# Kernel tuning notes

Hardware: AMD Instinct MI355X
Metric: run time of the kernel (lower is better)

Reference implementation:

```python
import jax, jax.numpy as jnp
import numpy as np

# ---- model / data constants ----
B, N, D, L = 32, 96, 64, 5          # graphs, nodes per graph, hidden, layers
EP = 768                             # directed edges per graph (symmetrized in to_dense)
NODE_VOCAB = 11                      # matches LocalFWL2(..., 11, 5, 'instance')
EDGE_VOCAB = 5                       # edge labels 0..4; index 5 = 'no edge' embedding row
EPS = 1e-5


def setup_inputs() -> dict:
    key = jax.random.key(0)
    ks = jax.random.split(key, 12)
    # block-contiguous batch: graph b owns nodes [b*N, (b+1)*N)
    x = jax.random.randint(ks[0], (B * N,), 0, NODE_VOCAB)
    u = jax.random.randint(ks[1], (B, EP), 0, N)
    v = jax.random.randint(ks[2], (B, EP), 0, N)
    off = (jnp.arange(B) * N)[:, None]
    edge_index = jnp.stack([(u + off).reshape(-1), (v + off).reshape(-1)], axis=0)
    edge_attr = jax.random.randint(ks[3], (B * EP,), 0, EDGE_VOCAB)
    s = 0.1
    inv = 1.0 / np.sqrt(D)
    return {
        "x": x,
        "edge_index": edge_index,
        "edge_attr": edge_attr,
        "node_emb": jax.random.normal(ks[4], (NODE_VOCAB, D), jnp.float32) * s,
        "edge_emb": jax.random.normal(ks[5], (EDGE_VOCAB + 1, D), jnp.float32) * s,
        "W1": jax.random.normal(ks[6], (L, D, D), jnp.float32) * inv,
        "b1": jnp.zeros((L, D), jnp.float32),
        "W2": jax.random.normal(ks[7], (L, D, D), jnp.float32) * inv,
        "b2": jnp.zeros((L, D), jnp.float32),
        "Wm": jax.random.normal(ks[8], (L, D, D), jnp.float32) * inv,
        "bm": jnp.zeros((L, D), jnp.float32),
        "gamma": jnp.ones((L, D), jnp.float32),
        "beta": jnp.zeros((L, D), jnp.float32),
        "pool_w": jax.random.normal(ks[9], (D, 1), jnp.float32) * inv,
        "pool_b": jnp.zeros((1,), jnp.float32),
    }


def reference(x, edge_index, edge_attr, node_emb, edge_emb,
              W1, b1, W2, b2, Wm, bm, gamma, beta, pool_w, pool_b):
    # ---- to_dense: sparse edge list -> dense per-graph edge-label matrix ----
    g = edge_index[0] // N
    u = edge_index[0] % N
    v = edge_index[1] % N
    A = jnp.full((B, N, N), EDGE_VOCAB, dtype=jnp.int32)        # EDGE_VOCAB = no-edge
    ea = edge_attr.astype(jnp.int32)
    A = A.at[g, u, v].set(ea)
    A = A.at[g, v, u].set(ea)                                    # undirected
    adj = (A != EDGE_VOCAB).astype(node_emb.dtype)               # [B,N,N]

    # ---- pair-state init: W_uv = h_u + h_v + edge_emb(A_uv) ----
    H = node_emb[x.reshape(B, N)]                                # [B,N,D]
    W = H[:, :, None, :] + H[:, None, :, :] + edge_emb[A]        # [B,N,N,D]

    # ---- local FWL(2) layers ----
    for l in range(L):
        h1 = jax.nn.relu(jnp.einsum('buwd,de->buwe', W, W1[l]) + b1[l])
        h2 = jax.nn.relu(jnp.einsum('bwvd,de->bwve', W, W2[l]) + b2[l])
        # aggregate over w restricted to neighbors of v (local FWL2)
        M = jnp.einsum('buwd,bwv,bwvd->buvd', h1, adj, h2)       # [B,N,N,D]
        W = W + jnp.einsum('buvd,de->buve', M, Wm[l]) + bm[l]
        # instance norm over the pair dims (u,v), per graph, per channel
        mu = W.mean(axis=(1, 2), keepdims=True)
        var = W.var(axis=(1, 2), keepdims=True)
        W = gamma[l] * (W - mu) * jax.lax.rsqrt(var + EPS) + beta[l]
        W = jax.nn.relu(W)

    # ---- pooling: sum over all pairs, then Linear(D, 1), squeeze ----
    pooled = W.sum(axis=(1, 2))                                  # [B,D]
    return (pooled @ pool_w + pool_b).squeeze(-1)                # [B]
```

## Files before the change

### kernel.cpp

```cpp
#include <hip/hip_runtime.h>
#include <hip/hip_bf16.h>

#define B_ 32
#define N_ 96
#define D_ 64
#define L_ 5
#define BE_ 24576
#define NN_ 9216
#define BNN_ 294912
#define EPS_ 1e-5f
#define INV_NN (1.0f/9216.0f)

typedef unsigned short u16;
typedef unsigned int u32;
typedef __attribute__((ext_vector_type(8))) short bf16x8;
typedef __attribute__((ext_vector_type(4))) float f32x4;

__device__ __forceinline__ float bf2f(u16 r){ return __uint_as_float(((u32)r) << 16); }
__device__ __forceinline__ u32 f2bf(float f){
  u32 u = __float_as_uint(f);
  return (u + 0x7fffu + ((u >> 16) & 1u)) >> 16;
}
__device__ __forceinline__ u32 pack2(float lo, float hi){
  return f2bf(lo) | (f2bf(hi) << 16);
}

__global__ void k_scatter(const int* __restrict__ ei, const int* __restrict__ ea,
                          int* __restrict__ A)
{
  int e = blockIdx.x * 256 + threadIdx.x;
  if (e >= BE_) return;
  int a = ei[e], bnode = ei[BE_ + e];
  int g = a / N_;
  int u = a % N_;
  int v = bnode % N_;
  int lab = ea[e] & 7;
  int base = g * NN_;
  atomicMax(&A[base + u * N_ + v], ((e + 1) << 3) | lab);
  atomicMax(&A[base + v * N_ + u], ((BE_ + e + 1) << 3) | lab);
}

__launch_bounds__(256)
__global__ void k_winit(const int* __restrict__ x, const int* __restrict__ A,
                        const float* __restrict__ nemb, const float* __restrict__ eemb,
                        u16* __restrict__ W)
{
  int gid = blockIdx.x * 256 + threadIdx.x;
  int d = (gid & 15) * 4;
  int p = gid >> 4;
  int b = p / NN_;
  int rem = p % NN_;
  int u = rem / N_;
  int v = rem % N_;
  int xu = x[b * N_ + u], xv = x[b * N_ + v];
  int pk = A[p];
  int lab = pk ? (pk & 7) : 5;
  float4 nu = *(const float4*)(nemb + xu * 64 + d);
  float4 nv = *(const float4*)(nemb + xv * 64 + d);
  float4 ee = *(const float4*)(eemb + lab * 64 + d);
  uint2 o;
  o.x = pack2(nu.x + nv.x + ee.x, nu.y + nv.y + ee.y);
  o.y = pack2(nu.z + nv.z + ee.z, nu.w + nv.w + ee.w);
  ((uint2*)W)[gid] = o;
}

__global__ void k_prep(const float* __restrict__ W1, const float* __restrict__ W2,
                       const float* __restrict__ Wm, u16* __restrict__ WT)
{
  int idx = blockIdx.x * 256 + threadIdx.x;
  if (idx >= 15 * 4096) return;
  int l3 = idx >> 12;
  int r  = idx & 4095;
  int e = r >> 6, d = r & 63;
  int l = l3 / 3, which = l3 % 3;
  const float* s = which == 0 ? W1 : which == 1 ? W2 : Wm;
  WT[idx] = (u16)f2bf(s[l * 4096 + d * 64 + e]);
}

__launch_bounds__(256)
__global__ void k_lin2(const u16* __restrict__ W, const u16* __restrict__ WT1,
                       const u16* __restrict__ WT2,
                       const float* __restrict__ b1l, const float* __restrict__ b2l,
                       const int* __restrict__ A,
                       const float* __restrict__ stp, const float* __restrict__ gml,
                       const float* __restrict__ btl,
                       int use_norm, u16* __restrict__ h1, u16* __restrict__ g2)
{
  __shared__ u16 Cs[64 * 136];
  __shared__ float nsS[128];
  const int tid = threadIdx.x;
  const int wave = tid >> 6, lane = tid & 63;
  const int lm = lane & 15, lg = lane >> 4;
  const int b = blockIdx.x / 72;
  const int qbase = (blockIdx.x % 72) * 128;

  if (use_norm) {
    if (tid < 128) nsS[tid] = stp[(size_t)b * 128 + tid];
    __syncthreads();
  }

  float sc[2][8], sh[2][8];
  if (use_norm) {
    #pragma unroll
    for (int s = 0; s < 2; ++s) {
      int d0 = s * 32 + lg * 8;
      #pragma unroll
      for (int j = 0; j < 8; ++j) {
        int d = d0 + j;
        float S1 = nsS[d], S2 = nsS[64 + d];
        float mu = S1 * INV_NN;
        float var = fmaf(S2, INV_NN, -mu * mu);
        float s0 = gml[d] * rsqrtf(var + EPS_);
        sc[s][j] = s0;
        sh[s][j] = fmaf(-mu, s0, btl[d]);
      }
    }
  } else {
    #pragma unroll
    for (int s = 0; s < 2; ++s)
      #pragma unroll
      for (int j = 0; j < 8; ++j) { sc[s][j] = 1.f; sh[s][j] = 0.f; }
  }

  bf16x8 bF[2][2];
  int flags[2];
  #pragma unroll
  for (int qt = 0; qt < 2; ++qt) {
    int q = qbase + wave * 32 + qt * 16 + lm;
    const u16* wrow = W + ((size_t)b * NN_ + q) * 64;
    flags[qt] = A[b * NN_ + q];
    #pragma unroll
    for (int s = 0; s < 2; ++s) {
      bf16x8 raw = *(const bf16x8*)(wrow + s * 32 + lg * 8);
      if (use_norm) {
        bf16x8 bb;
        #pragma unroll
        for (int j = 0; j < 8; ++j) {
          float v = bf2f((u16)raw[j]);
          v = fmaxf(fmaf(v, sc[s][j], sh[s][j]), 0.f);
          bb[j] = (short)f2bf(v);
        }
        bF[qt][s] = bb;
      } else {
        bF[qt][s] = raw;
      }
    }
  }

  const f32x4 zf = {0.f, 0.f, 0.f, 0.f};

  {
    bf16x8 aF[4][2];
    #pragma unroll
    for (int et = 0; et < 4; ++et)
      #pragma unroll
      for (int s = 0; s < 2; ++s)
        aF[et][s] = *(const bf16x8*)(WT1 + (et * 16 + lm) * 64 + s * 32 + lg * 8);
    float4 bsv[4];
    #pragma unroll
    for (int et = 0; et < 4; ++et) bsv[et] = *(const float4*)(b1l + et * 16 + lg * 4);
    #pragma unroll
    for (int qt = 0; qt < 2; ++qt) {
      f32x4 acc[4] = {zf, zf, zf, zf};
      #pragma unroll
      for (int s = 0; s < 2; ++s)
        #pragma unroll
        for (int et = 0; et < 4; ++et)
          acc[et] = __builtin_amdgcn_mfma_f32_16x16x32_bf16(aF[et][s], bF[qt][s], acc[et], 0, 0, 0);
      int col = wave * 32 + qt * 16 + lm;
      #pragma unroll
      for (int et = 0; et < 4; ++et) {
        float bv[4] = {bsv[et].x, bsv[et].y, bsv[et].z, bsv[et].w};
        #pragma unroll
        for (int r = 0; r < 4; ++r)
          Cs[(et * 16 + lg * 4 + r) * 136 + col] = (u16)f2bf(fmaxf(acc[et][r] + bv[r], 0.f));
      }
    }
  }
  __syncthreads();
  {
    u16* ob = h1 + (size_t)b * 64 * NN_ + qbase;
    for (int i = tid; i < 1024; i += 256) {
      int e = i >> 4, qc = (i & 15) * 8;
      uint4 val = *(const uint4*)&Cs[e * 136 + qc];
      *(uint4*)(ob + (size_t)e * NN_ + qc) = val;
    }
  }
  __syncthreads();

  {
    bf16x8 aF[4][2];
    #pragma unroll
    for (int et = 0; et < 4; ++et)
      #pragma unroll
      for (int s = 0; s < 2; ++s)
        aF[et][s] = *(const bf16x8*)(WT2 + (et * 16 + lm) * 64 + s * 32 + lg * 8);
    float4 bsv[4];
    #pragma unroll
    for (int et = 0; et < 4; ++et) bsv[et] = *(const float4*)(b2l + et * 16 + lg * 4);
    #pragma unroll
    for (int qt = 0; qt < 2; ++qt) {
      f32x4 acc[4] = {zf, zf, zf, zf};
      #pragma unroll
      for (int s = 0; s < 2; ++s)
        #pragma unroll
        for (int et = 0; et < 4; ++et)
          acc[et] = __builtin_amdgcn_mfma_f32_16x16x32_bf16(aF[et][s], bF[qt][s], acc[et], 0, 0, 0);
      int col = wave * 32 + qt * 16 + lm;
      #pragma unroll
      for (int et = 0; et < 4; ++et) {
        float bv[4] = {bsv[et].x, bsv[et].y, bsv[et].z, bsv[et].w};
        #pragma unroll
        for (int r = 0; r < 4; ++r) {
          float v = fmaxf(acc[et][r] + bv[r], 0.f);
          if (!flags[qt]) v = 0.f;
          Cs[(et * 16 + lg * 4 + r) * 136 + col] = (u16)f2bf(v);
        }
      }
    }
  }
  __syncthreads();
  {
    u16* ob = g2 + (size_t)b * 64 * NN_ + qbase;
    for (int i = tid; i < 1024; i += 256) {
      int e = i >> 4, qc = (i & 15) * 8;
      uint4 val = *(const uint4*)&Cs[e * 136 + qc];
      *(uint4*)(ob + (size_t)e * NN_ + qc) = val;
    }
  }
}

__launch_bounds__(256, 4)
__global__ void k_einsum(const u16* __restrict__ h1, const u16* __restrict__ g2n,
                         u16* __restrict__ M)
{
  __shared__ u32 Bt[96 * 60];
  u16* Cst = (u16*)Bt;
  const int tid = threadIdx.x;
  const int wave = tid >> 6, lane = tid & 63;
  const int lm = lane & 15, lg = lane >> 4;
  const int bd = blockIdx.x;
  const u16* h1p = h1 + (size_t)bd * NN_;
  const u16* g2p = g2n + (size_t)bd * NN_;
  const int u0 = (wave & 1) * 48, v0 = (wave >> 1) * 48;

  #pragma unroll
  for (int it = 0; it < 9; ++it) {
    int p = it * 256 + tid;
    int wp = p / 48, vh = (p % 48) * 2;
    u32 a = *(const u32*)(g2p + (2 * wp) * 96 + vh);
    u32 c = *(const u32*)(g2p + (2 * wp + 1) * 96 + vh);
    Bt[vh * 60 + wp]       = (a & 0xffffu) | (c << 16);
    Bt[(vh + 1) * 60 + wp] = (a >> 16) | (c & 0xffff0000u);
  }

  bf16x8 aF[3][3];
  #pragma unroll
  for (int t = 0; t < 3; ++t)
    #pragma unroll
    for (int s = 0; s < 3; ++s)
      aF[t][s] = *(const bf16x8*)(h1p + (u0 + t * 16 + lm) * 96 + s * 32 + lg * 8);
  __syncthreads();

  const f32x4 zf = {0.f, 0.f, 0.f, 0.f};
  f32x4 acc[3][3];
  #pragma unroll
  for (int i = 0; i < 3; ++i)
    #pragma unroll
    for (int j = 0; j < 3; ++j) acc[i][j] = zf;

  #pragma unroll
  for (int s = 0; s < 3; ++s) {
    bf16x8 bb[3];
    #pragma unroll
    for (int vt = 0; vt < 3; ++vt)
      bb[vt] = *(const bf16x8*)&Bt[(v0 + vt * 16 + lm) * 60 + s * 16 + lg * 4];
    #pragma unroll
    for (int ut = 0; ut < 3; ++ut)
      #pragma unroll
      for (int vt = 0; vt < 3; ++vt)
        acc[ut][vt] = __builtin_amdgcn_mfma_f32_16x16x32_bf16(aF[ut][s], bb[vt], acc[ut][vt], 0, 0, 0);
  }
  __syncthreads();

  #pragma unroll
  for (int ut = 0; ut < 3; ++ut)
    #pragma unroll
    for (int vt = 0; vt < 3; ++vt)
      #pragma unroll
      for (int r = 0; r < 4; ++r)
        Cst[(u0 + ut * 16 + lg * 4 + r) * 104 + v0 + vt * 16 + lm] = (u16)f2bf(acc[ut][vt][r]);
  __syncthreads();
  u16* Mp = M + (size_t)bd * NN_;
  for (int i = tid; i < 1152; i += 256) {
    int u = i / 12, vc = (i % 12) * 8;
    uint4 val = *(const uint4*)&Cst[u * 104 + vc];
    *(uint4*)(Mp + u * 96 + vc) = val;
  }
}

__launch_bounds__(128)
__global__ void k_update(const u16* __restrict__ M, const u16* __restrict__ WmT,
                         const float* __restrict__ bml, u16* __restrict__ W,
                         const float* __restrict__ stp, const float* __restrict__ gml,
                         const float* __restrict__ btl, int use_norm,
                         float* __restrict__ sto)
{
  __shared__ u16 Mt[64 * 64];
  __shared__ float red[2][128];
  __shared__ float nsS[128];
  const int tid = threadIdx.x;
  const int wave = tid >> 6, lane = tid & 63;
  const int lm = lane & 15, lg = lane >> 4;
  const int b = blockIdx.x / 144;
  const int qi = blockIdx.x % 144;
  const int qblk = qi * 64;

  if (use_norm) {
    if (tid < 128) nsS[tid] = stp[(size_t)b * 128 + tid];
  }

  bf16x8 aF[4][2];
  #pragma unroll
  for (int et = 0; et < 4; ++et)
    #pragma unroll
    for (int s = 0; s < 2; ++s)
      aF[et][s] = *(const bf16x8*)(WmT + (et * 16 + lm) * 64 + s * 32 + lg * 8);

  uint2 wres[2][4];
  #pragma unroll
  for (int qtL = 0; qtL < 2; ++qtL) {
    int qg = qblk + (wave * 2 + qtL) * 16 + lm;
    const u16* Wp = W + ((size_t)b * NN_ + qg) * 64;
    #pragma unroll
    for (int et = 0; et < 4; ++et)
      wres[qtL][et] = *(const uint2*)(Wp + et * 16 + lg * 4);
  }

  {
    const int dpl = tid >> 1;
    const int qob = tid & 1;
    const u16* Mb = M + (size_t)(b * 64 + dpl) * NN_ + qblk;
    #pragma unroll
    for (int t = 0; t < 4; ++t) {
      int qo = qob + t * 2;
      uint4 v = *(const uint4*)(Mb + qo * 8);
      u32 ws[4] = {v.x, v.y, v.z, v.w};
      #pragma unroll
      for (int h = 0; h < 4; ++h) {
        int j0 = h * 2;
        int q0 = qo * 8 + j0;
        int slot0 = (dpl >> 3) ^ j0 ^ (qo & 7);
        int slot1 = (dpl >> 3) ^ (j0 + 1) ^ (qo & 7);
        Mt[q0 * 64 + slot0 * 8 + (dpl & 7)]       = (u16)(ws[h] & 0xffffu);
        Mt[(q0 + 1) * 64 + slot1 * 8 + (dpl & 7)] = (u16)(ws[h] >> 16);
      }
    }
  }
  __syncthreads();

  float scn[4][4], shn[4][4];
  if (use_norm) {
    #pragma unroll
    for (int et = 0; et < 4; ++et) {
      int e0 = et * 16 + lg * 4;
      #pragma unroll
      for (int r = 0; r < 4; ++r) {
        int e = e0 + r;
        float S1 = nsS[e], S2 = nsS[64 + e];
        float mu = S1 * INV_NN;
        float var = fmaf(S2, INV_NN, -mu * mu);
        float s0 = gml[e] * rsqrtf(var + EPS_);
        scn[et][r] = s0;
        shn[et][r] = fmaf(-mu, s0, btl[e]);
      }
    }
  } else {
    #pragma unroll
    for (int et = 0; et < 4; ++et)
      #pragma unroll
      for (int r = 0; r < 4; ++r) { scn[et][r] = 1.f; shn[et][r] = 0.f; }
  }

  const f32x4 zf = {0.f, 0.f, 0.f, 0.f};
  f32x4 acc[2][4];
  #pragma unroll
  for (int i = 0; i < 2; ++i)
    #pragma unroll
    for (int j = 0; j < 4; ++j) acc[i][j] = zf;

  #pragma unroll
  for (int qtL = 0; qtL < 2; ++qtL) {
    int ql = (wave * 2 + qtL) * 16 + lm;
    bf16x8 bF[2];
    #pragma unroll
    for (int s = 0; s < 2; ++s) {
      int slot = (s * 4 + lg) ^ (ql & 7) ^ ((ql >> 3) & 7);
      bF[s] = *(const bf16x8*)&Mt[ql * 64 + slot * 8];
    }
    #pragma unroll
    for (int s = 0; s < 2; ++s)
      #pragma unroll
      for (int et = 0; et < 4; ++et)
        acc[qtL][et] = __builtin_amdgcn_mfma_f32_16x16x32_bf16(aF[et][s], bF[s], acc[qtL][et], 0, 0, 0);
  }

  float s1[4][4], s2[4][4];
  #pragma unroll
  for (int i = 0; i < 4; ++i)
    #pragma unroll
    for (int j = 0; j < 4; ++j) { s1[i][j] = 0.f; s2[i][j] = 0.f; }

  #pragma unroll
  for (int et = 0; et < 4; ++et) {
    int e0 = et * 16 + lg * 4;
    float4 bs = *(const float4*)(bml + e0);
    float bv[4] = {bs.x, bs.y, bs.z, bs.w};
    #pragma unroll
    for (int qtL = 0; qtL < 2; ++qtL) {
      int qg = qblk + (wave * 2 + qtL) * 16 + lm;
      u16* Wp = W + ((size_t)b * NN_ + qg) * 64 + e0;
      uint2 wo = wres[qtL][et];
      float wv[4] = {bf2f((u16)(wo.x & 0xffff)), bf2f((u16)(wo.x >> 16)),
                     bf2f((u16)(wo.y & 0xffff)), bf2f((u16)(wo.y >> 16))};
      float o[4];
      #pragma unroll
      for (int r = 0; r < 4; ++r) {
        float res = use_norm ? fmaxf(fmaf(wv[r], scn[et][r], shn[et][r]), 0.f) : wv[r];
        float val = acc[qtL][et][r] + bv[r] + res;
        o[r] = val;
        s1[et][r] += val;
        s2[et][r] = fmaf(val, val, s2[et][r]);
      }
      uint2 ov;
      ov.x = pack2(o[0], o[1]);
      ov.y = pack2(o[2], o[3]);
      *(uint2*)Wp = ov;
    }
  }

  #pragma unroll
  for (int et = 0; et < 4; ++et)
    #pragma unroll
    for (int r = 0; r < 4; ++r) {
      float a = s1[et][r], c = s2[et][r];
      a += __shfl_xor(a, 1, 64); a += __shfl_xor(a, 2, 64);
      a += __shfl_xor(a, 4, 64); a += __shfl_xor(a, 8, 64);
      c += __shfl_xor(c, 1, 64); c += __shfl_xor(c, 2, 64);
      c += __shfl_xor(c, 4, 64); c += __shfl_xor(c, 8, 64);
      if (lm == 0) {
        int e = et * 16 + lg * 4 + r;
        red[wave][e]      = a;
        red[wave][64 + e] = c;
      }
    }
  __syncthreads();
  if (tid < 128)
    atomicAdd(&sto[(size_t)b * 128 + tid], red[0][tid] + red[1][tid]);
}

__launch_bounds__(256)
__global__ void k_pool(const u16* __restrict__ W,
                       const float* __restrict__ stp,
                       const float* __restrict__ gml, const float* __restrict__ btl,
                       const float* __restrict__ pw, const float* __restrict__ pb,
                       float* __restrict__ out)
{
  __shared__ float nsS[128];
  const int b = blockIdx.x / 24;
  const int chunk = blockIdx.x % 24;
  const int tid = threadIdx.x;
  if (tid < 128) nsS[tid] = stp[(size_t)b * 128 + tid];
  __syncthreads();
  const int e = tid & 63;
  float S1 = nsS[e], S2 = nsS[64 + e];
  float mu = S1 * INV_NN;
  float var = fmaf(S2, INV_NN, -mu * mu);
  float rsig = rsqrtf(var + EPS_);
  float scl = gml[e] * rsig;
  float shf = fmaf(-mu, scl, btl[e]);
  float pwv = pw[e];
  const u16* base = W + (size_t)b * NN_ * 64 + chunk * 24576;
  float s = 0.f;
  for (int k = 0; k < 96; k++) {
    float w = bf2f(base[k * 256 + tid]);
    s += fmaxf(fmaf(w, scl, shf), 0.f) * pwv;
  }
  for (int o = 32; o; o >>= 1) s += __shfl_down(s, o, 64);
  __shared__ float rs[4];
  if ((tid & 63) == 0) rs[tid >> 6] = s;
  __syncthreads();
  if (tid == 0) {
    float t = rs[0] + rs[1] + rs[2] + rs[3];
    if (chunk == 0) t += pb[0];
    atomicAdd(&out[b], t);
  }
}

extern "C" void kernel_launch(void* const* d_in, const int* in_sizes, int n_in,
                              void* d_out, int out_size, void* d_ws, size_t ws_size,
                              hipStream_t stream) {
  const int*   x    = (const int*)d_in[0];
  const int*   ei   = (const int*)d_in[1];
  const int*   ea   = (const int*)d_in[2];
  const float* nemb = (const float*)d_in[3];
  const float* eemb = (const float*)d_in[4];
  const float* W1   = (const float*)d_in[5];
  const float* b1   = (const float*)d_in[6];
  const float* W2   = (const float*)d_in[7];
  const float* b2   = (const float*)d_in[8];
  const float* Wm   = (const float*)d_in[9];
  const float* bm   = (const float*)d_in[10];
  const float* gm   = (const float*)d_in[11];
  const float* bt   = (const float*)d_in[12];
  const float* pw   = (const float*)d_in[13];
  const float* pb   = (const float*)d_in[14];

  char* ws = (char*)d_ws;
  const size_t OFF_A  = 0;
  const size_t OFF_W  = 1179648;
  const size_t OFF_H1 = 38928384;
  const size_t OFF_G2 = 76677120;
  const size_t OFF_M  = 114425856;
  const size_t OFF_ST = 152174592;
  const size_t OFF_WT = 152256512;
  const size_t NEED   = OFF_WT + 122880;
  if (ws_size < NEED) return;

  int*   A     = (int*)(ws + OFF_A);
  u16*   W     = (u16*)(ws + OFF_W);
  u16*   h1    = (u16*)(ws + OFF_H1);
  u16*   g2n   = (u16*)(ws + OFF_G2);
  u16*   M     = (u16*)(ws + OFF_M);
  float* stats = (float*)(ws + OFF_ST);
  u16*   WT    = (u16*)(ws + OFF_WT);
  float* out   = (float*)d_out;

  hipMemsetAsync(A, 0, 1179648, stream);
  hipMemsetAsync(stats, 0, 81920, stream);
  hipMemsetAsync(out, 0, 32 * sizeof(float), stream);

  k_prep<<<240, 256, 0, stream>>>(W1, W2, Wm, WT);
  k_scatter<<<96, 256, 0, stream>>>(ei, ea, A);
  k_winit<<<18432, 256, 0, stream>>>(x, A, nemb, eemb, W);

  for (int l = 0; l < L_; l++) {
    int un = (l > 0);
    const float* stp = un ? stats + (size_t)(l - 1) * 4096 : stats;
    const float* gml = un ? gm + (l - 1) * 64 : gm;
    const float* btl = un ? bt + (l - 1) * 64 : bt;
    float* sto = stats + (size_t)l * 4096;
    k_lin2<<<2304, 256, 0, stream>>>(W, WT + (l * 3 + 0) * 4096, WT + (l * 3 + 1) * 4096,
                                     b1 + l * 64, b2 + l * 64, A, stp, gml, btl,
                                     un, h1, g2n);
    k_einsum<<<2048, 256, 0, stream>>>(h1, g2n, M);
    k_update<<<4608, 128, 0, stream>>>(M, WT + (l * 3 + 2) * 4096, bm + l * 64, W,
                                       stp, gml, btl, un, sto);
  }
  k_pool<<<768, 256, 0, stream>>>(W, stats + 4 * 4096, gm + 4 * 64, bt + 4 * 64,
                                  pw, pb, out);
}
```

Before: 621.7 us.

## Stage W and M tiles through LDS with coalesced loads; precompute norm scale/shift

k_update now loads the 64-row W tile into padded shared memory with coalesced 16-byte loads and writes it back coalesced, replacing strided per-lane 8-byte global reads and writes. The M transpose load is restructured so each thread reads four d-rows and packs pairs into 8-byte LDS stores rather than scalar 2-byte stores. Instance-norm scale and shift are computed once per graph in k_lin2 and stored to a small buffer that k_update reads directly. The cost is extra LDS use, which may reduce occupancy, plus a new cross-kernel dependency on the nsF buffer.

```diff
diff --git a/kernel.cpp b/kernel.cpp
--- a/kernel.cpp
+++ b/kernel.cpp
@@ -83,7 +83,7 @@
                        const float* __restrict__ b1l, const float* __restrict__ b2l,
                        const int* __restrict__ A,
                        const float* __restrict__ stp, const float* __restrict__ gml,
-                       const float* __restrict__ btl,
+                       const float* __restrict__ btl, float* __restrict__ nsF,
                        int use_norm, u16* __restrict__ h1, u16* __restrict__ g2)
 {
   __shared__ u16 Cs[64 * 136];
@@ -114,6 +114,14 @@
         sc[s][j] = s0;
         sh[s][j] = fmaf(-mu, s0, btl[d]);
       }
+    }
+    if ((blockIdx.x % 72) == 0 && tid < 64) {
+      float S1 = nsS[tid], S2 = nsS[64 + tid];
+      float mu = S1 * INV_NN;
+      float var = fmaf(S2, INV_NN, -mu * mu);
+      float s0 = gml[tid] * rsqrtf(var + EPS_);
+      nsF[((size_t)b * 64 + tid) * 2]     = s0;
+      nsF[((size_t)b * 64 + tid) * 2 + 1] = fmaf(-mu, s0, btl[tid]);
     }
   } else {
     #pragma unroll
@@ -302,13 +310,12 @@
 __launch_bounds__(128)
 __global__ void k_update(const u16* __restrict__ M, const u16* __restrict__ WmT,
                          const float* __restrict__ bml, u16* __restrict__ W,
-                         const float* __restrict__ stp, const float* __restrict__ gml,
-                         const float* __restrict__ btl, int use_norm,
+                         const float* __restrict__ nsF, int use_norm,
                          float* __restrict__ sto)
 {
   __shared__ u16 Mt[64 * 64];
+  __shared__ u16 Ws[64 * 80];
   __shared__ float red[2][128];
-  __shared__ float nsS[128];
   const int tid = threadIdx.x;
   const int wave = tid >> 6, lane = tid & 63;
   const int lm = lane & 15, lg = lane >> 4;
@@ -316,10 +323,6 @@
   const int qi = blockIdx.x % 144;
   const int qblk = qi * 64;
 
-  if (use_norm) {
-    if (tid < 128) nsS[tid] = stp[(size_t)b * 128 + tid];
-  }
-
   bf16x8 aF[4][2];
   #pragma unroll
   for (int et = 0; et < 4; ++et)
@@ -327,53 +330,15 @@
     for (int s = 0; s < 2; ++s)
       aF[et][s] = *(const bf16x8*)(WmT + (et * 16 + lm) * 64 + s * 32 + lg * 8);
 
-  uint2 wres[2][4];
-  #pragma unroll
-  for (int qtL = 0; qtL < 2; ++qtL) {
-    int qg = qblk + (wave * 2 + qtL) * 16 + lm;
-    const u16* Wp = W + ((size_t)b * NN_ + qg) * 64;
-    #pragma unroll
-    for (int et = 0; et < 4; ++et)
-      wres[qtL][et] = *(const uint2*)(Wp + et * 16 + lg * 4);
-  }
-
-  {
-    const int dpl = tid >> 1;
-    const int qob = tid & 1;
-    const u16* Mb = M + (size_t)(b * 64 + dpl) * NN_ + qblk;
-    #pragma unroll
-    for (int t = 0; t < 4; ++t) {
-      int qo = qob + t * 2;
-      uint4 v = *(const uint4*)(Mb + qo * 8);
-      u32 ws[4] = {v.x, v.y, v.z, v.w};
-      #pragma unroll
-      for (int h = 0; h < 4; ++h) {
-        int j0 = h * 2;
-        int q0 = qo * 8 + j0;
-        int slot0 = (dpl >> 3) ^ j0 ^ (qo & 7);
-        int slot1 = (dpl >> 3) ^ (j0 + 1) ^ (qo & 7);
-        Mt[q0 * 64 + slot0 * 8 + (dpl & 7)]       = (u16)(ws[h] & 0xffffu);
-        Mt[(q0 + 1) * 64 + slot1 * 8 + (dpl & 7)] = (u16)(ws[h] >> 16);
-      }
-    }
-  }
-  __syncthreads();
-
   float scn[4][4], shn[4][4];
   if (use_norm) {
     #pragma unroll
     for (int et = 0; et < 4; ++et) {
       int e0 = et * 16 + lg * 4;
-      #pragma unroll
-      for (int r = 0; r < 4; ++r) {
-        int e = e0 + r;
-        float S1 = nsS[e], S2 = nsS[64 + e];
-        float mu = S1 * INV_NN;
-        float var = fmaf(S2, INV_NN, -mu * mu);
-        float s0 = gml[e] * rsqrtf(var + EPS_);
-        scn[et][r] = s0;
-        shn[et][r] = fmaf(-mu, s0, btl[e]);
-      }
+      float4 t0 = *(const float4*)(nsF + ((size_t)b * 64 + e0) * 2);
+      float4 t1 = *(const float4*)(nsF + ((size_t)b * 64 + e0) * 2 + 4);
+      scn[et][0] = t0.x; shn[et][0] = t0.y; scn[et][1] = t0.z; shn[et][1] = t0.w;
+      scn[et][2] = t1.x; shn[et][2] = t1.y; scn[et][3] = t1.z; shn[et][3] = t1.w;
     }
   } else {
     #pragma unroll
@@ -381,6 +346,45 @@
       #pragma unroll
       for (int r = 0; r < 4; ++r) { scn[et][r] = 1.f; shn[et][r] = 0.f; }
   }
+
+  {
+    const int rw = tid >> 3, c8 = tid & 7;
+    const u16* Wb = W + ((size_t)b * NN_ + qblk) * 64;
+    #pragma unroll
+    for (int t = 0; t < 4; ++t) {
+      int q = rw + t * 16;
+      uint4 v = *(const uint4*)(Wb + (size_t)q * 64 + c8 * 8);
+      *(uint4*)&Ws[q * 80 + c8 * 8] = v;
+    }
+  }
+
+  {
+    const int pg = tid >> 3;
+    const int oc = tid & 7;
+    const u16* Mb = M + (size_t)(b * 64) * NN_ + qblk + oc * 8;
+    uint4 v[4];
+    #pragma unroll
+    for (int t = 0; t < 4; ++t)
+      v[t] = *(const uint4*)(Mb + (size_t)(pg * 4 + t) * NN_);
+    const int dg = pg >> 1;
+    const int dh = (pg & 1) * 4;
+    const u32* p0 = (const u32*)&v[0];
+    const u32* p1 = (const u32*)&v[1];
+    const u32* p2 = (const u32*)&v[2];
+    const u32* p3 = (const u32*)&v[3];
+    #pragma unroll
+    for (int j = 0; j < 8; ++j) {
+      u32 a0 = p0[j >> 1], a1 = p1[j >> 1], a2 = p2[j >> 1], a3 = p3[j >> 1];
+      u32 w0, w1;
+      if (j & 1) { w0 = (a0 >> 16) | (a1 & 0xffff0000u); w1 = (a2 >> 16) | (a3 & 0xffff0000u); }
+      else       { w0 = (a0 & 0xffffu) | (a1 << 16);     w1 = (a2 & 0xffffu) | (a3 << 16); }
+      int q = oc * 8 + j;
+      int slot = dg ^ j ^ oc;
+      uint2 wv; wv.x = w0; wv.y = w1;
+      *(uint2*)&Mt[q * 64 + slot * 8 + dh] = wv;
+    }
+  }
+  __syncthreads();
 
   const f32x4 zf = {0.f, 0.f, 0.f, 0.f};
   f32x4 acc[2][4];
@@ -418,9 +422,9 @@
     float bv[4] = {bs.x, bs.y, bs.z, bs.w};
     #pragma unroll
     for (int qtL = 0; qtL < 2; ++qtL) {
-      int qg = qblk + (wave * 2 + qtL) * 16 + lm;
-      u16* Wp = W + ((size_t)b * NN_ + qg) * 64 + e0;
-      uint2 wo = wres[qtL][et];
+      int ql = (wave * 2 + qtL) * 16 + lm;
+      u16* Wp = &Ws[ql * 80 + e0];
+      uint2 wo = *(const uint2*)Wp;
       float wv[4] = {bf2f((u16)(wo.x & 0xffff)), bf2f((u16)(wo.x >> 16)),
                      bf2f((u16)(wo.y & 0xffff)), bf2f((u16)(wo.y >> 16))};
       float o[4];
@@ -455,6 +459,17 @@
       }
     }
   __syncthreads();
+
+  {
+    const int rw = tid >> 3, c8 = tid & 7;
+    u16* Wb = W + ((size_t)b * NN_ + qblk) * 64;
+    #pragma unroll
+    for (int t = 0; t < 4; ++t) {
+      int q = rw + t * 16;
+      uint4 v = *(const uint4*)&Ws[q * 80 + c8 * 8];
+      *(uint4*)(Wb + (size_t)q * 64 + c8 * 8) = v;
+    }
+  }
   if (tid < 128)
     atomicAdd(&sto[(size_t)b * 128 + tid], red[0][tid] + red[1][tid]);
 }
@@ -523,7 +538,8 @@
   const size_t OFF_G2 = 76677120;
   const size_t OFF_M  = 114425856;
   const size_t OFF_ST = 152174592;
-  const size_t OFF_WT = 152256512;
+  const size_t OFF_NF = 152256512;
+  const size_t OFF_WT = 152272896;
   const size_t NEED   = OFF_WT + 122880;
   if (ws_size < NEED) return;
 
@@ -533,6 +549,7 @@
   u16*   g2n   = (u16*)(ws + OFF_G2);
   u16*   M     = (u16*)(ws + OFF_M);
   float* stats = (float*)(ws + OFF_ST);
+  float* nsF   = (float*)(ws + OFF_NF);
   u16*   WT    = (u16*)(ws + OFF_WT);
   float* out   = (float*)d_out;
 
@@ -551,11 +568,11 @@
     const float* btl = un ? bt + (l - 1) * 64 : bt;
     float* sto = stats + (size_t)l * 4096;
     k_lin2<<<2304, 256, 0, stream>>>(W, WT + (l * 3 + 0) * 4096, WT + (l * 3 + 1) * 4096,
-                                     b1 + l * 64, b2 + l * 64, A, stp, gml, btl,
+                                     b1 + l * 64, b2 + l * 64, A, stp, gml, btl, nsF,
                                      un, h1, g2n);
     k_einsum<<<2048, 256, 0, stream>>>(h1, g2n, M);
     k_update<<<4608, 128, 0, stream>>>(M, WT + (l * 3 + 2) * 4096, bm + l * 64, W,
-                                       stp, gml, btl, un, sto);
+                                       nsF, un, sto);
   }
   k_pool<<<768, 256, 0, stream>>>(W, stats + 4 * 4096, gm + 4 * 64, bt + 4 * 64,
                                   pw, pb, out);
```

Result: no change. 616.5 us (-0.8%).
